# Optimization experiments

Hardware: AMD Instinct MI355X
Metric: run time of the kernel (lower is better)

## Reference

```python
import jax, jax.numpy as jnp
import numpy as np
from jax import lax

HEADS = 8
WIN_SIZES = (2, 4, 8)


def _linear(x, w, b):
    return x @ w + b


def _window_attention(x2d, ws, w4, b4):
    # x2d: (B,H,W,C); w4: (4,C,C) = [q,k,v,out]; b4: (4,C)
    B, H, W, C = x2d.shape
    p1, p2 = H // ws, W // ws
    xw = x2d.reshape(B, p1, ws, p2, ws, C).transpose(0, 1, 3, 2, 4, 5)
    xw = xw.reshape(B, p1, p2, ws * ws, C)
    hs = C // HEADS
    q = _linear(xw, w4[0], b4[0]).reshape(B, p1, p2, ws * ws, HEADS, hs)
    k = _linear(xw, w4[1], b4[1]).reshape(B, p1, p2, ws * ws, HEADS, hs)
    v = _linear(xw, w4[2], b4[2]).reshape(B, p1, p2, ws * ws, HEADS, hs)
    scores = jnp.einsum('bpqwhd,bpqvhd->bpqhwv', q, k) / jnp.sqrt(jnp.asarray(hs, x2d.dtype))
    probs = jax.nn.softmax(scores, axis=-1)
    ctx = jnp.einsum('bpqhwv,bpqvhd->bpqwhd', probs, v).reshape(B, p1, p2, ws * ws, C)
    return _linear(ctx, w4[3], b4[3])


def _unwindow(out, ws):
    B, p1, p2, win, C = out.shape
    s = out.reshape(B, p1, p2, ws, ws, C).transpose(0, 1, 3, 2, 4, 5)
    return s.reshape(B, p1 * ws, p2 * ws, C)


def _up_bilinear_ac(x, oh, ow):
    # x: (B,C,h,w); bilinear with align_corners=True (UpsamplingBilinear2d)
    B, C, h, w = x.shape
    def grid(o, i):
        pos = jnp.arange(o, dtype=x.dtype) * ((i - 1) / (o - 1))
        i0 = jnp.floor(pos).astype(jnp.int32)
        i1 = jnp.minimum(i0 + 1, i - 1)
        return i0, i1, pos - i0.astype(x.dtype)
    r0, r1, tr = grid(oh, h)
    c0, c1, tc = grid(ow, w)
    xr = x[:, :, r0, :] * (1 - tr)[None, None, :, None] + x[:, :, r1, :] * tr[None, None, :, None]
    return xr[:, :, :, c0] * (1 - tc) + xr[:, :, :, c1] * tc


def _forward(x, attn_w, attn_b, edge_w, mlp_w1, mlp_b1, mlp_w2, mlp_b2,
             dl_w, dl_b, ax_w, ax_b, g_shift, g_bias, sq_w, sq_b):
    B, N, C = x.shape
    H = W = int(np.sqrt(N))
    x2d = x.reshape(B, H, W, C)

    # multi-scale window attention branches
    scale_outputs = [_unwindow(_window_attention(x2d, ws, attn_w[i], attn_b[i]), ws)
                     for i, ws in enumerate(WIN_SIZES)]

    # adaptive window selector
    xc = x2d.transpose(0, 3, 1, 2)  # (B,C,H,W)
    edge = jnp.abs(lax.conv_general_dilated(xc, edge_w, (1, 1), 'SAME'))
    avg = lax.reduce_window(edge, 0.0, lax.add, (1, 1, 3, 3), (1, 1, 1, 1), 'SAME') / 9.0
    e = avg.transpose(0, 2, 3, 1)  # (B,H,W,1)
    wts = jax.nn.softmax(jax.nn.relu(e @ mlp_w1 + mlp_b1) @ mlp_w2 + mlp_b2, axis=-1)

    blended = sum(wts[..., i:i + 1] * scale_outputs[i] for i in range(len(WIN_SIZES)))
    h_map = blended.transpose(0, 3, 1, 2)  # (B,C,H,W)

    # ws=4 window attention -> DlightConv token pooling
    x_win = _window_attention(x2d, 4, attn_w[1], attn_b[1])  # (B,p,p,16,C)
    probs = jax.nn.softmax(jnp.mean(x_win, axis=-2) @ dl_w + dl_b, axis=-1)
    x_dl = jnp.sum(x_win * probs[..., None], axis=-2)  # (B,p,p,C)

    # axial attention (no head split, no scaling in the axial branch)
    q = _linear(x_dl, ax_w[0], ax_b[0])
    k = _linear(x_dl, ax_w[1], ax_b[1])
    v = _linear(x_dl, ax_w[2], ax_b[2])
    scores_x = jnp.einsum('bhwc,bhvc->bhwv', q, k)  # (B,r,c,k)
    scores_y = jnp.einsum('bhwc,bvwc->bwhv', q, k)  # (B,c,r,k)

    # GaussianTrans: vectorized per-pixel gaussian positional bias
    p = x_dl.shape[1]
    idx = jnp.arange(p, dtype=x.dtype)
    dist2 = (idx[None, :] - idx[:, None]) ** 2          # [pos, k]
    gb = -(g_shift[0] * dist2 + g_bias[0])              # (p,p)
    ax = jax.nn.softmax(scores_x + gb[None, None, :, :], axis=-1)       # bias indexed by c
    ay = jax.nn.softmax(jnp.swapaxes(scores_y, 1, 2) + gb[None, :, None, :], axis=-1)  # bias by r
    x_g = jnp.einsum('brck,brkd->brcd', ax, v) + jnp.einsum('brck,bkcd->brcd', ay, v)

    x_g = _up_bilinear_ac(x_g.transpose(0, 3, 1, 2), H, W)  # (B,C,H,W)

    cat = jnp.concatenate([x_g, h_map], axis=1)  # (B,2C,H,W)
    out = jnp.einsum('oc,bchw->bohw', sq_w, cat) + sq_b[None, :, None, None]
    return out.transpose(0, 2, 3, 1).reshape(B, N, C)


def setup_inputs() -> dict:
    key = jax.random.key(0)
    ks = jax.random.split(key, 16)
    B, N, C = 16, 4096, 256
    s = 0.02
    return {
        'x': jax.random.normal(ks[0], (B, N, C), jnp.float32),
        'attn_w': jax.random.normal(ks[1], (3, 4, C, C), jnp.float32) * s,
        'attn_b': jax.random.normal(ks[2], (3, 4, C), jnp.float32) * s,
        'edge_w': jax.random.normal(ks[3], (1, C, 3, 3), jnp.float32) * s,
        'mlp_w1': jax.random.normal(ks[4], (1, 16), jnp.float32) * s,
        'mlp_b1': jax.random.normal(ks[5], (16,), jnp.float32) * s,
        'mlp_w2': jax.random.normal(ks[6], (16, 3), jnp.float32) * s,
        'mlp_b2': jax.random.normal(ks[7], (3,), jnp.float32) * s,
        'dl_w': jax.random.normal(ks[8], (C, 16), jnp.float32) * s,
        'dl_b': jax.random.normal(ks[9], (16,), jnp.float32) * s,
        'ax_w': jax.random.normal(ks[10], (3, C, C), jnp.float32) * s,
        'ax_b': jax.random.normal(ks[11], (3, C), jnp.float32) * s,
        'g_shift': jnp.abs(jax.random.normal(ks[12], (1,), jnp.float32)),
        'g_bias': -jnp.abs(jax.random.normal(ks[13], (1,), jnp.float32)),
        'sq_w': jax.random.normal(ks[14], (C, 2 * C), jnp.float32) * s,
        'sq_b': jax.random.normal(ks[15], (C,), jnp.float32) * s,
    }


def reference(x, attn_w, attn_b, edge_w, mlp_w1, mlp_b1, mlp_w2, mlp_b2,
              dl_w, dl_b, ax_w, ax_b, g_shift, g_bias, sq_w, sq_b):
    return _forward(x, attn_w, attn_b, edge_w, mlp_w1, mlp_b1, mlp_w2, mlp_b2,
                    dl_w, dl_b, ax_w, ax_b, g_shift, g_bias, sq_w, sq_b)
```

## Files before the change

kernel.cpp:

```cpp
#include <hip/hip_runtime.h>
#include <math.h>


#define CHUNK_B 4
#define CHUNK_TOK (CHUNK_B * 4096)
#define SA 40

typedef __attribute__((ext_vector_type(8))) short short8;
typedef __attribute__((ext_vector_type(4))) float f32x4;

__device__ __forceinline__ ushort f2bf(float f) {
    union { float f; unsigned u; } v; v.f = f;
    unsigned r = v.u + 0x7fff + ((v.u >> 16) & 1);
    return (ushort)(r >> 16);
}
__device__ __forceinline__ float bf2f(ushort h) {
    union { unsigned u; float f; } v; v.u = ((unsigned)h) << 16; return v.f;
}
__device__ __forceinline__ void split2(float v, ushort& h, ushort& l) {
    h = f2bf(v);
    l = f2bf(v - bf2f(h));
}

__global__ __launch_bounds__(256) void split_w_kmajor(
    const float* __restrict__ W, ushort* __restrict__ Th, ushort* __restrict__ Tl, int nmats)
{
    const int idx = blockIdx.x * 256 + threadIdx.x;
    if (idx >= nmats * 65536) return;
    const int mat = idx >> 16, r = idx & 65535;
    const int n = r >> 8, k = r & 255;
    const float v = W[(size_t)mat * 65536 + k * 256 + n];
    ushort h, l; split2(v, h, l);
    Th[idx] = h; Tl[idx] = l;
}
__global__ __launch_bounds__(256) void split_w_nmajor(
    const float* __restrict__ W, ushort* __restrict__ Th, ushort* __restrict__ Tl, int total)
{
    const int idx = blockIdx.x * 256 + threadIdx.x;
    if (idx >= total) return;
    ushort h, l; split2(W[idx], h, l);
    Th[idx] = h; Tl[idx] = l;
}

#define GEMM_DECLS                                                            \
    __shared__ ushort Ah[128 * SA], Al[128 * SA], Bh[128 * SA], Bl[128 * SA]; \
    const int tid = threadIdx.x;                                              \
    const int wave = tid >> 6, lane = tid & 63;                               \
    const int quad = lane >> 4, l16 = lane & 15;                              \
    const int wr = (wave >> 1) * 64, wc = (wave & 1) * 64;                    \
    f32x4 acc[4][4];                                                          \
    _Pragma("unroll") for (int i = 0; i < 4; i++)                             \
        _Pragma("unroll") for (int j = 0; j < 4; j++)                         \
            acc[i][j] = (f32x4){0.f, 0.f, 0.f, 0.f};                          \
    const int srow = tid >> 1;                                    \
    const int skp  = (tid & 1) * 16;

#define STAGE_A(Aptr, kk)                                                     \
    {                                                                         \
        const float* src = (Aptr) + (size_t)(m0 + srow) * 256 + (kk) + skp;   \
        _Pragma("unroll") for (int c = 0; c < 4; c++) {                       \
            float4 v = *(const float4*)(src + c * 4);                         \
            ushort4 h, l;                                                     \
            split2(v.x, h.x, l.x); split2(v.y, h.y, l.y);                     \
            split2(v.z, h.z, l.z); split2(v.w, h.w, l.w);                     \
            *(ushort4*)&Ah[srow * SA + skp + c * 4] = h;                      \
            *(ushort4*)&Al[srow * SA + skp + c * 4] = l;                      \
        }                                                                     \
    }

#define STAGE_B(WthP, WtlP, Kst, k0)                                          \
    {                                                                         \
        const size_t wo = (size_t)(srow) * (Kst) + (k0) + skp;                \
        *(ulonglong2*)&Bh[srow * SA + skp]     = *(const ulonglong2*)((WthP) + wo);     \
        *(ulonglong2*)&Bh[srow * SA + skp + 8] = *(const ulonglong2*)((WthP) + wo + 8); \
        *(ulonglong2*)&Bl[srow * SA + skp]     = *(const ulonglong2*)((WtlP) + wo);     \
        *(ulonglong2*)&Bl[srow * SA + skp + 8] = *(const ulonglong2*)((WtlP) + wo + 8); \
    }

#define GEMM_COMPUTE                                                          \
    {                                                                         \
        short8 afh[4], afl[4], bfh[4], bfl[4];                                \
        _Pragma("unroll") for (int i = 0; i < 4; i++) {                       \
            const int ro = (wr + i * 16 + l16) * SA + quad * 8;               \
            afh[i] = *(const short8*)&Ah[ro];                                 \
            afl[i] = *(const short8*)&Al[ro];                                 \
        }                                                                     \
        _Pragma("unroll") for (int j = 0; j < 4; j++) {                       \
            const int no = (wc + j * 16 + l16) * SA + quad * 8;               \
            bfh[j] = *(const short8*)&Bh[no];                                 \
            bfl[j] = *(const short8*)&Bl[no];                                 \
        }                                                                     \
        _Pragma("unroll") for (int i = 0; i < 4; i++)                         \
            _Pragma("unroll") for (int j = 0; j < 4; j++) {                   \
                acc[i][j] = __builtin_amdgcn_mfma_f32_16x16x32_bf16(          \
                    afh[i], bfh[j], acc[i][j], 0, 0, 0);                      \
                acc[i][j] = __builtin_amdgcn_mfma_f32_16x16x32_bf16(          \
                    afl[i], bfh[j], acc[i][j], 0, 0, 0);                      \
                acc[i][j] = __builtin_amdgcn_mfma_f32_16x16x32_bf16(          \
                    afh[i], bfl[j], acc[i][j], 0, 0, 0);                      \
            }                                                                 \
    }

__global__ __launch_bounds__(256, 2) void gemm3_mfma(
    const float* __restrict__ A,
    const ushort* __restrict__ Wth, const ushort* __restrict__ Wtl,
    const float* __restrict__ b0, const float* __restrict__ b1, const float* __restrict__ b2,
    float* __restrict__ O0, float* __restrict__ O1, float* __restrict__ O2)
{
    const int m0 = blockIdx.x * 128;
    const int mat = blockIdx.y >> 1;
    const int col0 = (blockIdx.y & 1) * 128;
    const ushort* wth = Wth + (size_t)mat * 65536 + (size_t)col0 * 256;
    const ushort* wtl = Wtl + (size_t)mat * 65536 + (size_t)col0 * 256;
    GEMM_DECLS
    for (int k0 = 0; k0 < 256; k0 += 32) {
        STAGE_A(A, k0)
        STAGE_B(wth, wtl, 256, k0)
        __syncthreads();
        GEMM_COMPUTE
        __syncthreads();
    }
    const float* bias = (mat == 0) ? b0 : (mat == 1) ? b1 : b2;
    float* O = (mat == 0) ? O0 : (mat == 1) ? O1 : O2;
#pragma unroll
    for (int j = 0; j < 4; j++) {
        const int col = col0 + wc + j * 16 + l16;
        const float bj = bias[col];
#pragma unroll
        for (int i = 0; i < 4; i++) {
            const int rbase = m0 + wr + i * 16 + quad * 4;
#pragma unroll
            for (int r = 0; r < 4; r++)
                O[(size_t)(rbase + r) * 256 + col] = acc[i][j][r] + bj;
        }
    }
}

__global__ __launch_bounds__(256, 2) void gemmp_mfma(
    const float* __restrict__ A,
    const ushort* __restrict__ Wth, const ushort* __restrict__ Wtl,
    const float* __restrict__ bias,
    float* __restrict__ Sout, int store_s,
    float* __restrict__ Blnd, const float* __restrict__ wts, int scale_idx, int blend_init,
    int row_off)
{
    const int m0 = blockIdx.x * 128;
    const int col0 = blockIdx.y * 128;
    const ushort* wth = Wth + (size_t)col0 * 256;
    const ushort* wtl = Wtl + (size_t)col0 * 256;
    GEMM_DECLS
    for (int k0 = 0; k0 < 256; k0 += 32) {
        STAGE_A(A, k0)
        STAGE_B(wth, wtl, 256, k0)
        __syncthreads();
        GEMM_COMPUTE
        __syncthreads();
    }
#pragma unroll
    for (int i = 0; i < 4; i++) {
        const int rbase = m0 + wr + i * 16 + quad * 4;
#pragma unroll
        for (int r = 0; r < 4; r++) {
            const size_t grow = (size_t)row_off + rbase + r;
            const float wt = wts[grow * 3 + scale_idx];
#pragma unroll
            for (int j = 0; j < 4; j++) {
                const int col = col0 + wc + j * 16 + l16;
                const float v = acc[i][j][r] + bias[col];
                if (store_s) Sout[grow * 256 + col] = v;
                float* bp = Blnd + grow * 256 + col;
                if (blend_init) *bp = wt * v;
                else            *bp = *bp + wt * v;
            }
        }
    }
}

__global__ __launch_bounds__(256, 2) void gemmf_mfma(
    const float* __restrict__ UP, const float* __restrict__ BLD,
    const ushort* __restrict__ Wth, const ushort* __restrict__ Wtl,
    const float* __restrict__ SQB, float* __restrict__ OUT)
{
    const int m0 = blockIdx.x * 128;
    const int col0 = blockIdx.y * 128;
    const ushort* wth = Wth + (size_t)col0 * 512;
    const ushort* wtl = Wtl + (size_t)col0 * 512;
    GEMM_DECLS
    for (int k0 = 0; k0 < 512; k0 += 32) {
        const float* Ap = (k0 < 256) ? UP : BLD;
        STAGE_A(Ap, (k0 & 255))
        STAGE_B(wth, wtl, 512, k0)
        __syncthreads();
        GEMM_COMPUTE
        __syncthreads();
    }
#pragma unroll
    for (int j = 0; j < 4; j++) {
        const int col = col0 + wc + j * 16 + l16;
        const float bj = SQB[col];
#pragma unroll
        for (int i = 0; i < 4; i++) {
            const int rbase = m0 + wr + i * 16 + quad * 4;
#pragma unroll
            for (int r = 0; r < 4; r++)
                OUT[(size_t)(rbase + r) * 256 + col] = acc[i][j][r] + bj;
        }
    }
}

template <int WS, int NH>
__global__ __launch_bounds__(256) void win_attn(
    const float* __restrict__ Q, const float* __restrict__ K,
    const float* __restrict__ V, float* __restrict__ CTX)
{
    constexpr int WIN = WS * WS;
    constexpr int NW = 64 / WS;
    constexpr int CW = NH * 32;
    __shared__ float qs[WIN][CW + 4], ks[WIN][CW + 4], vs[WIN][CW + 4];
    __shared__ float sc[NH][WIN][WIN + 1];
    const int tid = threadIdx.x;
    const int wid = blockIdx.x;
    const int b = wid / (NW * NW);
    const int rem = wid % (NW * NW);
    const int p = rem / NW, q = rem % NW;
    const int h0 = blockIdx.y * NH;

    for (int idx = tid; idx < WIN * CW; idx += 256) {
        const int i = idx / CW;
        const int cc = idx % CW;
        const int ti = i / WS, tj = i % WS;
        const size_t g = ((size_t)(b * 4096 + (p * WS + ti) * 64 + (q * WS + tj))) * 256 + h0 * 32 + cc;
        qs[i][cc] = Q[g]; ks[i][cc] = K[g]; vs[i][cc] = V[g];
    }
    __syncthreads();
    const float scale = 0.17677669529663687f;
    for (int idx = tid; idx < NH * WIN * WIN; idx += 256) {
        const int hl = idx / (WIN * WIN);
        const int r = idx % (WIN * WIN);
        const int i = r / WIN, j = r % WIN;
        const int co = hl * 32;
        float s = 0.f;
#pragma unroll
        for (int d = 0; d < 32; d++) s += qs[i][co + d] * ks[j][co + d];
        sc[hl][i][j] = s * scale;
    }
    __syncthreads();
    if (tid < NH * WIN) {
        const int hl = tid / WIN, i = tid % WIN;
        float mx = -3.4e38f;
        for (int j = 0; j < WIN; j++) mx = fmaxf(mx, sc[hl][i][j]);
        float sum = 0.f;
        for (int j = 0; j < WIN; j++) {
            float e = __expf(sc[hl][i][j] - mx);
            sc[hl][i][j] = e; sum += e;
        }
        const float inv = 1.f / sum;
        for (int j = 0; j < WIN; j++) sc[hl][i][j] *= inv;
    }
    __syncthreads();
    for (int idx = tid; idx < WIN * CW; idx += 256) {
        const int i = idx / CW;
        const int cc = idx % CW;
        const int hl = cc >> 5;
        float s = 0.f;
        for (int j = 0; j < WIN; j++) s += sc[hl][i][j] * vs[j][cc];
        const int ti = i / WS, tj = i % WS;
        const size_t g = ((size_t)(b * 4096 + (p * WS + ti) * 64 + (q * WS + tj))) * 256 + h0 * 32 + cc;
        CTX[g] = s;
    }
}

__global__ __launch_bounds__(256) void edge_gemm9(
    const float* __restrict__ x, const float* __restrict__ ew, float* __restrict__ ytmp)
{
    __shared__ float wsm[2304];
    const int tid = threadIdx.x;
    for (int i = tid; i < 2304; i += 256) wsm[i] = ew[i];
    __syncthreads();
    const int wave = tid >> 6, lane = tid & 63;
    const int p = blockIdx.x * 4 + wave;
    const float4 xv = *(const float4*)(x + (size_t)p * 256 + lane * 4);
    float acc[9];
#pragma unroll
    for (int t = 0; t < 9; t++) acc[t] = 0.f;
    const float xs[4] = {xv.x, xv.y, xv.z, xv.w};
#pragma unroll
    for (int i = 0; i < 4; i++) {
        const int c = lane * 4 + i;
#pragma unroll
        for (int t = 0; t < 9; t++)
            acc[t] = fmaf(xs[i], wsm[c * 9 + t], acc[t]);
    }
#pragma unroll
    for (int t = 0; t < 9; t++) {
#pragma unroll
        for (int off = 1; off < 64; off <<= 1)
            acc[t] += __shfl_xor(acc[t], off);
    }
    if (lane < 9) {
        float v = acc[0];
        switch (lane) {
            case 1: v = acc[1]; break; case 2: v = acc[2]; break;
            case 3: v = acc[3]; break; case 4: v = acc[4]; break;
            case 5: v = acc[5]; break; case 6: v = acc[6]; break;
            case 7: v = acc[7]; break; case 8: v = acc[8]; break;
            default: break;
        }
        ytmp[(size_t)p * 9 + lane] = v;
    }
}

__global__ __launch_bounds__(256) void edge_combine(
    const float* __restrict__ ytmp, float* __restrict__ edge)
{
    const int idx = blockIdx.x * 256 + threadIdx.x;
    const int b = idx >> 12, rem = idx & 4095, h = rem >> 6, w = rem & 63;
    float s = 0.f;
#pragma unroll
    for (int kh = 0; kh < 3; kh++) {
        const int hh = h + kh - 1;
        if ((unsigned)hh > 63u) continue;
#pragma unroll
        for (int kw = 0; kw < 3; kw++) {
            const int ww = w + kw - 1;
            if ((unsigned)ww > 63u) continue;
            s += ytmp[((size_t)b * 4096 + hh * 64 + ww) * 9 + kh * 3 + kw];
        }
    }
    edge[idx] = fabsf(s);
}

__global__ __launch_bounds__(256) void avg_mlp(
    const float* __restrict__ edge, const float* __restrict__ w1, const float* __restrict__ b1,
    const float* __restrict__ w2, const float* __restrict__ b2, float* __restrict__ wts)
{
    const int idx = blockIdx.x * 256 + threadIdx.x;
    const int b = idx >> 12, rem = idx & 4095, h = rem >> 6, w = rem & 63;
    float s = 0.f;
#pragma unroll
    for (int kh = -1; kh <= 1; kh++) {
        const int hh = h + kh;
        if ((unsigned)hh > 63u) continue;
#pragma unroll
        for (int kw = -1; kw <= 1; kw++) {
            const int ww = w + kw;
            if ((unsigned)ww > 63u) continue;
            s += edge[(size_t)b * 4096 + hh * 64 + ww];
        }
    }
    const float e = s / 9.f;
    float l0 = b2[0], l1 = b2[1], l2 = b2[2];
#pragma unroll
    for (int j = 0; j < 16; j++) {
        float hd = fmaxf(e * w1[j] + b1[j], 0.f);
        l0 += hd * w2[j * 3 + 0];
        l1 += hd * w2[j * 3 + 1];
        l2 += hd * w2[j * 3 + 2];
    }
    const float mx = fmaxf(l0, fmaxf(l1, l2));
    const float e0 = __expf(l0 - mx), e1 = __expf(l1 - mx), e2 = __expf(l2 - mx);
    const float inv = 1.f / (e0 + e1 + e2);
    wts[(size_t)idx * 3 + 0] = e0 * inv;
    wts[(size_t)idx * 3 + 1] = e1 * inv;
    wts[(size_t)idx * 3 + 2] = e2 * inv;
}

__global__ __launch_bounds__(256) void dlight(
    const float* __restrict__ S1, const float* __restrict__ dlw,
    const float* __restrict__ dlb, float* __restrict__ XDL)
{
    __shared__ float xw[16][257];
    __shared__ float m[256];
    __shared__ float pr[16];
    __shared__ float pr2[16];
    const int wid = blockIdx.x;
    const int b = wid >> 8, rem = wid & 255, p = rem >> 4, q = rem & 15;
    const int tid = threadIdx.x;
#pragma unroll
    for (int t = 0; t < 16; t++) {
        const int ti = t >> 2, tj = t & 3;
        xw[t][tid] = S1[((size_t)b * 4096 + (p * 4 + ti) * 64 + (q * 4 + tj)) * 256 + tid];
    }
    float mm = 0.f;
#pragma unroll
    for (int t = 0; t < 16; t++) mm += xw[t][tid];
    m[tid] = mm * (1.f / 16.f);
    __syncthreads();
    if (tid < 16) {
        float lg = dlb[tid];
        for (int c = 0; c < 256; c++) lg += m[c] * dlw[c * 16 + tid];
        pr[tid] = lg;
    }
    __syncthreads();
    if (tid < 16) {
        float mx = -3.4e38f;
        for (int j = 0; j < 16; j++) mx = fmaxf(mx, pr[j]);
        float sum = 0.f;
        for (int j = 0; j < 16; j++) sum += __expf(pr[j] - mx);
        pr2[tid] = __expf(pr[tid] - mx) / sum;
    }
    __syncthreads();
    float o = 0.f;
#pragma unroll
    for (int t = 0; t < 16; t++) o += xw[t][tid] * pr2[t];
    XDL[(size_t)wid * 256 + tid] = o;
}

__global__ __launch_bounds__(256) void axial_row(
    const float* __restrict__ Q, const float* __restrict__ K, const float* __restrict__ V,
    const float* __restrict__ gsp, const float* __restrict__ gbp, float* __restrict__ XG)
{
    __shared__ float qs[16][257], ks[16][257], vs[16][257];
    __shared__ float sc[16][17];
    const int bid = blockIdx.x;
    const int b = bid >> 4, r = bid & 15;
    const int tid = threadIdx.x;
    const float gs = gsp[0], gb = gbp[0];
#pragma unroll
    for (int w = 0; w < 16; w++) {
        const size_t base = ((size_t)b * 256 + r * 16 + w) * 256 + tid;
        qs[w][tid] = Q[base]; ks[w][tid] = K[base]; vs[w][tid] = V[base];
    }
    __syncthreads();
    {
        const int w = tid >> 4, vv = tid & 15;
        float s = 0.f;
        for (int c = 0; c < 256; c++) s += qs[w][c] * ks[vv][c];
        const float d = (float)(w - vv);
        sc[w][vv] = s - (gs * d * d + gb);
    }
    __syncthreads();
    if (tid < 16) {
        float mx = -3.4e38f;
        for (int j = 0; j < 16; j++) mx = fmaxf(mx, sc[tid][j]);
        float sum = 0.f;
        for (int j = 0; j < 16; j++) {
            float e = __expf(sc[tid][j] - mx);
            sc[tid][j] = e; sum += e;
        }
        const float inv = 1.f / sum;
        for (int j = 0; j < 16; j++) sc[tid][j] *= inv;
    }
    __syncthreads();
#pragma unroll
    for (int w2 = 0; w2 < 16; w2++) {
        float o = 0.f;
#pragma unroll
        for (int k2 = 0; k2 < 16; k2++) o += sc[w2][k2] * vs[k2][tid];
        XG[((size_t)b * 256 + r * 16 + w2) * 256 + tid] = o;
    }
}

__global__ __launch_bounds__(256) void axial_col(
    const float* __restrict__ Q, const float* __restrict__ K, const float* __restrict__ V,
    const float* __restrict__ gsp, const float* __restrict__ gbp, float* __restrict__ XG)
{
    __shared__ float qs[16][257], ks[16][257], vs[16][257];
    __shared__ float sc[16][17];
    const int bid = blockIdx.x;
    const int b = bid >> 4, col = bid & 15;
    const int tid = threadIdx.x;
    const float gs = gsp[0], gb = gbp[0];
#pragma unroll
    for (int h = 0; h < 16; h++) {
        const size_t base = ((size_t)b * 256 + h * 16 + col) * 256 + tid;
        qs[h][tid] = Q[base]; ks[h][tid] = K[base]; vs[h][tid] = V[base];
    }
    __syncthreads();
    {
        const int r = tid >> 4, vv = tid & 15;
        float s = 0.f;
        for (int c = 0; c < 256; c++) s += qs[r][c] * ks[vv][c];
        const float d = (float)(r - vv);
        sc[r][vv] = s - (gs * d * d + gb);
    }
    __syncthreads();
    if (tid < 16) {
        float mx = -3.4e38f;
        for (int j = 0; j < 16; j++) mx = fmaxf(mx, sc[tid][j]);
        float sum = 0.f;
        for (int j = 0; j < 16; j++) {
            float e = __expf(sc[tid][j] - mx);
            sc[tid][j] = e; sum += e;
        }
        const float inv = 1.f / sum;
        for (int j = 0; j < 16; j++) sc[tid][j] *= inv;
    }
    __syncthreads();
#pragma unroll
    for (int r2 = 0; r2 < 16; r2++) {
        float o = 0.f;
#pragma unroll
        for (int k2 = 0; k2 < 16; k2++) o += sc[r2][k2] * vs[k2][tid];
        XG[((size_t)b * 256 + r2 * 16 + col) * 256 + tid] += o;
    }
}

__global__ __launch_bounds__(256) void upsample(
    const float* __restrict__ XG, float* __restrict__ UP)
{
    const unsigned idx = blockIdx.x * 256u + threadIdx.x;
    const int c = idx & 255;
    const unsigned t2 = idx >> 8;
    const int w = t2 & 63;
    const unsigned t3 = t2 >> 6;
    const int h = t3 & 63;
    const int b = t3 >> 6;
    const float rr = 15.f / 63.f;
    const float ph = h * rr, pw = w * rr;
    int h0 = (int)floorf(ph); float th = ph - (float)h0; int h1 = min(h0 + 1, 15);
    int w0 = (int)floorf(pw); float tw = pw - (float)w0; int w1 = min(w0 + 1, 15);
    const size_t bb = (size_t)b * 256;
    const float v00 = XG[((bb + h0 * 16 + w0)) * 256 + c];
    const float v10 = XG[((bb + h1 * 16 + w0)) * 256 + c];
    const float v01 = XG[((bb + h0 * 16 + w1)) * 256 + c];
    const float v11 = XG[((bb + h1 * 16 + w1)) * 256 + c];
    const float c0 = v00 * (1.f - th) + v10 * th;
    const float c1 = v01 * (1.f - th) + v11 * th;
    UP[idx] = c0 * (1.f - tw) + c1 * tw;
}

extern "C" void kernel_launch(void* const* d_in, const int* in_sizes, int n_in,
                              void* d_out, int out_size, void* d_ws, size_t ws_size,
                              hipStream_t stream)
{
    const float* x      = (const float*)d_in[0];
    const float* attn_w = (const float*)d_in[1];
    const float* attn_b = (const float*)d_in[2];
    const float* edge_w = (const float*)d_in[3];
    const float* mlp_w1 = (const float*)d_in[4];
    const float* mlp_b1 = (const float*)d_in[5];
    const float* mlp_w2 = (const float*)d_in[6];
    const float* mlp_b2 = (const float*)d_in[7];
    const float* dl_w   = (const float*)d_in[8];
    const float* dl_b   = (const float*)d_in[9];
    const float* ax_w   = (const float*)d_in[10];
    const float* ax_b   = (const float*)d_in[11];
    const float* g_shift= (const float*)d_in[12];
    const float* g_bias = (const float*)d_in[13];
    const float* sq_w   = (const float*)d_in[14];
    const float* sq_b   = (const float*)d_in[15];
    float* out = (float*)d_out;

    float* ws = (float*)d_ws;
    const size_t MT = 65536;
    float* blend = ws;
    float* s1    = blend + MT * 256;
    float* scr   = s1 + MT * 256;
    float* chQ   = scr;
    float* chK   = chQ + (size_t)CHUNK_TOK * 256;
    float* chV   = chK + (size_t)CHUNK_TOK * 256;
    float* up    = scr;
    float* ytmp  = scr;
    float* edge  = scr + MT * 256;
    float* wts   = edge + 65536;
    float* xdl   = wts + 196608;
    float* axq   = xdl + 1048576;
    float* axk   = axq + 1048576;
    float* axv   = axk + 1048576;
    float* xg    = axv + 1048576;
    ushort* Wth = (ushort*)(xg + 1048576);
    ushort* Wtl = Wth + 1114112;

    split_w_kmajor<<<(12 * 65536 + 255) / 256, 256, 0, stream>>>(attn_w, Wth, Wtl, 12);
    split_w_kmajor<<<(3 * 65536 + 255) / 256, 256, 0, stream>>>(
        ax_w, Wth + (size_t)12 * 65536, Wtl + (size_t)12 * 65536, 3);
    split_w_nmajor<<<(131072 + 255) / 256, 256, 0, stream>>>(
        sq_w, Wth + (size_t)15 * 65536, Wtl + (size_t)15 * 65536, 131072);

    edge_gemm9<<<16384, 256, 0, stream>>>(x, edge_w, ytmp);
    edge_combine<<<256, 256, 0, stream>>>(ytmp, edge);
    avg_mlp<<<256, 256, 0, stream>>>(edge, mlp_w1, mlp_b1, mlp_w2, mlp_b2, wts);

    for (int i = 0; i < 3; i++) {
        const ushort* Wh = Wth + (size_t)i * 4 * 65536;
        const ushort* Wl = Wtl + (size_t)i * 4 * 65536;
        const float* c0 = attn_b + (size_t)(i * 4 + 0) * 256;
        const float* c1 = attn_b + (size_t)(i * 4 + 1) * 256;
        const float* c2 = attn_b + (size_t)(i * 4 + 2) * 256;
        const float* c3 = attn_b + (size_t)(i * 4 + 3) * 256;
        for (int ch = 0; ch < 16 / CHUNK_B; ch++) {
            const size_t toff = (size_t)ch * CHUNK_TOK;
            const float* xc = x + toff * 256;
            gemm3_mfma<<<dim3(CHUNK_TOK / 128, 6), 256, 0, stream>>>(
                xc, Wh, Wl, c0, c1, c2, chQ, chK, chV);
            if (i == 0)
                win_attn<2, 8><<<dim3(CHUNK_B * 32 * 32, 1), 256, 0, stream>>>(chQ, chK, chV, chQ);
            if (i == 1)
                win_attn<4, 4><<<dim3(CHUNK_B * 16 * 16, 2), 256, 0, stream>>>(chQ, chK, chV, chQ);
            if (i == 2)
                win_attn<8, 1><<<dim3(CHUNK_B * 8 * 8, 8), 256, 0, stream>>>(chQ, chK, chV, chQ);
            gemmp_mfma<<<dim3(CHUNK_TOK / 128, 2), 256, 0, stream>>>(
                chQ, Wh + (size_t)3 * 65536, Wl + (size_t)3 * 65536, c3,
                s1, (i == 1) ? 1 : 0, blend, wts, i, (i == 0) ? 1 : 0, (int)toff);
        }
    }

    dlight<<<4096, 256, 0, stream>>>(s1, dl_w, dl_b, xdl);

    gemm3_mfma<<<dim3(4096 / 128, 6), 256, 0, stream>>>(
        xdl, Wth + (size_t)12 * 65536, Wtl + (size_t)12 * 65536,
        ax_b, ax_b + 256, ax_b + 512, axq, axk, axv);
    axial_row<<<256, 256, 0, stream>>>(axq, axk, axv, g_shift, g_bias, xg);
    axial_col<<<256, 256, 0, stream>>>(axq, axk, axv, g_shift, g_bias, xg);

    upsample<<<65536, 256, 0, stream>>>(xg, up);

    gemmf_mfma<<<dim3(512, 2), 256, 0, stream>>>(
        up, blend, Wth + (size_t)15 * 65536, Wtl + (size_t)15 * 65536, sq_b, out);
}
```

Before: 1.306 ms.

## Stage GEMM tiles via direct global-to-LDS loads and pre-split bf16 producers

Replaces register-staged loads of the weight tiles with global_load_lds direct-to-LDS copies, and removes the padded LDS stride (SA 40 to KS 32). Producer kernels (window attention context and upsample) now emit pre-split bf16 hi/lo pairs, so the projection and final GEMMs can stage A through direct LDS loads instead of converting fp32 on the fly. The aim is to cut VGPR traffic and conversion work in the GEMM inner loops. The unpadded LDS layout may add bank conflicts on fragment reads. Writing hi/lo halves is the same number of bytes as fp32 but goes to separate arrays, and it needs extra workspace for the ctx buffers.

```diff
diff --git a/kernel.cpp b/kernel.cpp
--- a/kernel.cpp
+++ b/kernel.cpp
@@ -4,9 +4,10 @@
 
 #define CHUNK_B 4
 #define CHUNK_TOK (CHUNK_B * 4096)
-#define SA 40
+#define KS 32
 
 typedef __attribute__((ext_vector_type(8))) short short8;
+typedef __attribute__((ext_vector_type(8))) unsigned short ushort8;
 typedef __attribute__((ext_vector_type(4))) float f32x4;
 
 __device__ __forceinline__ ushort f2bf(float f) {
@@ -20,6 +21,13 @@
 __device__ __forceinline__ void split2(float v, ushort& h, ushort& l) {
     h = f2bf(v);
     l = f2bf(v - bf2f(h));
+}
+
+__device__ __forceinline__ void gld16(const ushort* g, ushort* l) {
+    __builtin_amdgcn_global_load_lds(
+        (const __attribute__((address_space(1))) unsigned int*)g,
+        (__attribute__((address_space(3))) unsigned int*)l,
+        16, 0, 0);
 }
 
 __global__ __launch_bounds__(256) void split_w_kmajor(
@@ -43,7 +51,7 @@
 }
 
 #define GEMM_DECLS                                                            \
-    __shared__ ushort Ah[128 * SA], Al[128 * SA], Bh[128 * SA], Bl[128 * SA]; \
+    __shared__ ushort Ah[128 * KS], Al[128 * KS], Bh[128 * KS], Bl[128 * KS]; \
     const int tid = threadIdx.x;                                              \
     const int wave = tid >> 6, lane = tid & 63;                               \
     const int quad = lane >> 4, l16 = lane & 15;                              \
@@ -55,38 +63,43 @@
     const int srow = tid >> 1;                                    \
     const int skp  = (tid & 1) * 16;
 
-#define STAGE_A(Aptr, kk)                                                     \
+#define STAGE_GLD(dstbuf, srcp, strideE, rowbase, k0e)                        \
+    _Pragma("unroll") for (int jj = 0; jj < 2; jj++) {                        \
+        const int rr = (wave << 5) + (jj << 4) + (lane >> 2);                 \
+        gld16((srcp) + (size_t)((rowbase) + rr) * (strideE) + (k0e) + ((lane & 3) << 3), \
+              (dstbuf) + (wave << 10) + (jj << 9));                           \
+    }
+
+#define STAGE_A_SPLIT(Aptr, kk)                                               \
     {                                                                         \
-        const float* src = (Aptr) + (size_t)(m0 + srow) * 256 + (kk) + skp;   \
-        _Pragma("unroll") for (int c = 0; c < 4; c++) {                       \
-            float4 v = *(const float4*)(src + c * 4);                         \
-            ushort4 h, l;                                                     \
-            split2(v.x, h.x, l.x); split2(v.y, h.y, l.y);                     \
-            split2(v.z, h.z, l.z); split2(v.w, h.w, l.w);                     \
-            *(ushort4*)&Ah[srow * SA + skp + c * 4] = h;                      \
-            *(ushort4*)&Al[srow * SA + skp + c * 4] = l;                      \
+        const float* srcp = (Aptr) + (size_t)(m0 + srow) * 256 + (kk) + skp;  \
+        _Pragma("unroll") for (int c = 0; c < 2; c++) {                       \
+            float4 v0 = *(const float4*)(srcp + c * 8);                       \
+            float4 v1 = *(const float4*)(srcp + c * 8 + 4);                   \
+            ushort8 h, l; ushort hh, ll;                                      \
+            split2(v0.x, hh, ll); h[0] = hh; l[0] = ll;                       \
+            split2(v0.y, hh, ll); h[1] = hh; l[1] = ll;                       \
+            split2(v0.z, hh, ll); h[2] = hh; l[2] = ll;                       \
+            split2(v0.w, hh, ll); h[3] = hh; l[3] = ll;                       \
+            split2(v1.x, hh, ll); h[4] = hh; l[4] = ll;                       \
+            split2(v1.y, hh, ll); h[5] = hh; l[5] = ll;                       \
+            split2(v1.z, hh, ll); h[6] = hh; l[6] = ll;                       \
+            split2(v1.w, hh, ll); h[7] = hh; l[7] = ll;                       \
+            *(ushort8*)&Ah[srow * KS + skp + c * 8] = h;                      \
+            *(ushort8*)&Al[srow * KS + skp + c * 8] = l;                      \
         }                                                                     \
-    }
-
-#define STAGE_B(WthP, WtlP, Kst, k0)                                          \
-    {                                                                         \
-        const size_t wo = (size_t)(srow) * (Kst) + (k0) + skp;                \
-        *(ulonglong2*)&Bh[srow * SA + skp]     = *(const ulonglong2*)((WthP) + wo);     \
-        *(ulonglong2*)&Bh[srow * SA + skp + 8] = *(const ulonglong2*)((WthP) + wo + 8); \
-        *(ulonglong2*)&Bl[srow * SA + skp]     = *(const ulonglong2*)((WtlP) + wo);     \
-        *(ulonglong2*)&Bl[srow * SA + skp + 8] = *(const ulonglong2*)((WtlP) + wo + 8); \
     }
 
 #define GEMM_COMPUTE                                                          \
     {                                                                         \
         short8 afh[4], afl[4], bfh[4], bfl[4];                                \
         _Pragma("unroll") for (int i = 0; i < 4; i++) {                       \
-            const int ro = (wr + i * 16 + l16) * SA + quad * 8;               \
+            const int ro = (wr + i * 16 + l16) * KS + quad * 8;               \
             afh[i] = *(const short8*)&Ah[ro];                                 \
             afl[i] = *(const short8*)&Al[ro];                                 \
         }                                                                     \
         _Pragma("unroll") for (int j = 0; j < 4; j++) {                       \
-            const int no = (wc + j * 16 + l16) * SA + quad * 8;               \
+            const int no = (wc + j * 16 + l16) * KS + quad * 8;               \
             bfh[j] = *(const short8*)&Bh[no];                                 \
             bfl[j] = *(const short8*)&Bl[no];                                 \
         }                                                                     \
@@ -114,8 +127,9 @@
     const ushort* wtl = Wtl + (size_t)mat * 65536 + (size_t)col0 * 256;
     GEMM_DECLS
     for (int k0 = 0; k0 < 256; k0 += 32) {
-        STAGE_A(A, k0)
-        STAGE_B(wth, wtl, 256, k0)
+        STAGE_GLD(Bh, wth, 256, 0, k0)
+        STAGE_GLD(Bl, wtl, 256, 0, k0)
+        STAGE_A_SPLIT(A, k0)
         __syncthreads();
         GEMM_COMPUTE
         __syncthreads();
@@ -137,7 +151,7 @@
 }
 
 __global__ __launch_bounds__(256, 2) void gemmp_mfma(
-    const float* __restrict__ A,
+    const ushort* __restrict__ AgH, const ushort* __restrict__ AgL,
     const ushort* __restrict__ Wth, const ushort* __restrict__ Wtl,
     const float* __restrict__ bias,
     float* __restrict__ Sout, int store_s,
@@ -149,9 +163,12 @@
     const ushort* wth = Wth + (size_t)col0 * 256;
     const ushort* wtl = Wtl + (size_t)col0 * 256;
     GEMM_DECLS
+    (void)srow; (void)skp;
     for (int k0 = 0; k0 < 256; k0 += 32) {
-        STAGE_A(A, k0)
-        STAGE_B(wth, wtl, 256, k0)
+        STAGE_GLD(Ah, AgH, 256, m0, k0)
+        STAGE_GLD(Al, AgL, 256, m0, k0)
+        STAGE_GLD(Bh, wth, 256, 0, k0)
+        STAGE_GLD(Bl, wtl, 256, 0, k0)
         __syncthreads();
         GEMM_COMPUTE
         __syncthreads();
@@ -177,7 +194,8 @@
 }
 
 __global__ __launch_bounds__(256, 2) void gemmf_mfma(
-    const float* __restrict__ UP, const float* __restrict__ BLD,
+    const ushort* __restrict__ UPH, const ushort* __restrict__ UPL,
+    const float* __restrict__ BLD,
     const ushort* __restrict__ Wth, const ushort* __restrict__ Wtl,
     const float* __restrict__ SQB, float* __restrict__ OUT)
 {
@@ -187,9 +205,14 @@
     const ushort* wtl = Wtl + (size_t)col0 * 512;
     GEMM_DECLS
     for (int k0 = 0; k0 < 512; k0 += 32) {
-        const float* Ap = (k0 < 256) ? UP : BLD;
-        STAGE_A(Ap, (k0 & 255))
-        STAGE_B(wth, wtl, 512, k0)
+        STAGE_GLD(Bh, wth, 512, 0, k0)
+        STAGE_GLD(Bl, wtl, 512, 0, k0)
+        if (k0 < 256) {
+            STAGE_GLD(Ah, UPH, 256, m0, k0)
+            STAGE_GLD(Al, UPL, 256, m0, k0)
+        } else {
+            STAGE_A_SPLIT(BLD, (k0 & 255))
+        }
         __syncthreads();
         GEMM_COMPUTE
         __syncthreads();
@@ -211,7 +234,7 @@
 template <int WS, int NH>
 __global__ __launch_bounds__(256) void win_attn(
     const float* __restrict__ Q, const float* __restrict__ K,
-    const float* __restrict__ V, float* __restrict__ CTX)
+    const float* __restrict__ V, ushort* __restrict__ CTXh, ushort* __restrict__ CTXl)
 {
     constexpr int WIN = WS * WS;
     constexpr int NW = 64 / WS;
@@ -266,7 +289,8 @@
         for (int j = 0; j < WIN; j++) s += sc[hl][i][j] * vs[j][cc];
         const int ti = i / WS, tj = i % WS;
         const size_t g = ((size_t)(b * 4096 + (p * WS + ti) * 64 + (q * WS + tj))) * 256 + h0 * 32 + cc;
-        CTX[g] = s;
+        ushort hh, ll; split2(s, hh, ll);
+        CTXh[g] = hh; CTXl[g] = ll;
     }
 }
 
@@ -497,7 +521,7 @@
 }
 
 __global__ __launch_bounds__(256) void upsample(
-    const float* __restrict__ XG, float* __restrict__ UP)
+    const float* __restrict__ XG, ushort* __restrict__ UPH, ushort* __restrict__ UPL)
 {
     const unsigned idx = blockIdx.x * 256u + threadIdx.x;
     const int c = idx & 255;
@@ -517,7 +541,9 @@
     const float v11 = XG[((bb + h1 * 16 + w1)) * 256 + c];
     const float c0 = v00 * (1.f - th) + v10 * th;
     const float c1 = v01 * (1.f - th) + v11 * th;
-    UP[idx] = c0 * (1.f - tw) + c1 * tw;
+    const float val = c0 * (1.f - tw) + c1 * tw;
+    ushort hh, ll; split2(val, hh, ll);
+    UPH[idx] = hh; UPL[idx] = ll;
 }
 
 extern "C" void kernel_launch(void* const* d_in, const int* in_sizes, int n_in,
@@ -550,7 +576,10 @@
     float* chQ   = scr;
     float* chK   = chQ + (size_t)CHUNK_TOK * 256;
     float* chV   = chK + (size_t)CHUNK_TOK * 256;
-    float* up    = scr;
+    ushort* ctxh = (ushort*)(chV + (size_t)CHUNK_TOK * 256);
+    ushort* ctxl = ctxh + (size_t)CHUNK_TOK * 256;
+    ushort* uph  = (ushort*)scr;
+    ushort* upl  = uph + MT * 256;
     float* ytmp  = scr;
     float* edge  = scr + MT * 256;
     float* wts   = edge + 65536;
@@ -585,13 +614,13 @@
             gemm3_mfma<<<dim3(CHUNK_TOK / 128, 6), 256, 0, stream>>>(
                 xc, Wh, Wl, c0, c1, c2, chQ, chK, chV);
             if (i == 0)
-                win_attn<2, 8><<<dim3(CHUNK_B * 32 * 32, 1), 256, 0, stream>>>(chQ, chK, chV, chQ);
+                win_attn<2, 8><<<dim3(CHUNK_B * 32 * 32, 1), 256, 0, stream>>>(chQ, chK, chV, ctxh, ctxl);
             if (i == 1)
-                win_attn<4, 4><<<dim3(CHUNK_B * 16 * 16, 2), 256, 0, stream>>>(chQ, chK, chV, chQ);
+                win_attn<4, 4><<<dim3(CHUNK_B * 16 * 16, 2), 256, 0, stream>>>(chQ, chK, chV, ctxh, ctxl);
             if (i == 2)
-                win_attn<8, 1><<<dim3(CHUNK_B * 8 * 8, 8), 256, 0, stream>>>(chQ, chK, chV, chQ);
+                win_attn<8, 1><<<dim3(CHUNK_B * 8 * 8, 8), 256, 0, stream>>>(chQ, chK, chV, ctxh, ctxl);
             gemmp_mfma<<<dim3(CHUNK_TOK / 128, 2), 256, 0, stream>>>(
-                chQ, Wh + (size_t)3 * 65536, Wl + (size_t)3 * 65536, c3,
+                ctxh, ctxl, Wh + (size_t)3 * 65536, Wl + (size_t)3 * 65536, c3,
                 s1, (i == 1) ? 1 : 0, blend, wts, i, (i == 0) ? 1 : 0, (int)toff);
         }
     }
@@ -604,8 +633,8 @@
     axial_row<<<256, 256, 0, stream>>>(axq, axk, axv, g_shift, g_bias, xg);
     axial_col<<<256, 256, 0, stream>>>(axq, axk, axv, g_shift, g_bias, xg);
 
-    upsample<<<65536, 256, 0, stream>>>(xg, up);
+    upsample<<<65536, 256, 0, stream>>>(xg, uph, upl);
 
     gemmf_mfma<<<dim3(512, 2), 256, 0, stream>>>(
-        up, blend, Wth + (size_t)15 * 65536, Wtl + (size_t)15 * 65536, sq_b, out);
-}
+        uph, upl, blend, Wth + (size_t)15 * 65536, Wtl + (size_t)15 * 65536, sq_b, out);
+}
```

Result: no change. 1.296 ms (-0.8%).
